# Performance work log

Measured on AMD Instinct MI355X. Metric: run time of the kernel, lower is better.

Reference implementation:

```python
import jax, jax.numpy as jnp
import numpy as np

NUM_HEADS = 16
D_MODEL = 2048
HEAD_DIM = 128
ROPE_BASE = 10000


def setup_inputs() -> dict:
    key = jax.random.key(0)
    k1, k2, k3 = jax.random.split(key, 3)
    B, S = 2, 2048
    x = jax.random.normal(k1, (B, S, D_MODEL), dtype=jnp.float32)
    attn_mask = jnp.ones((B, S), dtype=jnp.int32)
    in_proj = 0.02 * jax.random.normal(k2, (3, D_MODEL, NUM_HEADS, HEAD_DIM), dtype=jnp.float32)
    out_proj = 0.02 * jax.random.normal(k3, (NUM_HEADS, HEAD_DIM, D_MODEL), dtype=jnp.float32)
    return {"x": x, "attn_mask": attn_mask, "in_proj": in_proj, "out_proj": out_proj}


def _rope(t, seq_len):
    # t: [B, S, H, hd]; faithful to RotaryEmbedding.__call__ (concat layout, not interleaved)
    half = HEAD_DIM // 2
    inv_freq = 1.0 / (ROPE_BASE ** (2 * jnp.arange(0, half, dtype=jnp.float32) / HEAD_DIM))
    positions = jnp.arange(seq_len, dtype=jnp.float32)
    angles = positions[:, None] * inv_freq[None, :]            # [S, hd/2]
    cos = jnp.cos(angles)[None, :, None, :]                    # [1, S, 1, hd/2]
    sin = jnp.sin(angles)[None, :, None, :]
    tr = t.reshape(*t.shape[:-1], half, 2)                     # [B,S,H,hd/2,2]
    t0, t1 = tr[..., 0], tr[..., 1]
    out = jnp.concatenate([t0 * cos - t1 * sin, t0 * sin + t1 * cos], axis=-1)
    return out.reshape(t.shape)


def reference(x, attn_mask, in_proj, out_proj):
    B, S, D = x.shape
    qkv = jnp.einsum('bsd,tdhm->tbshm', x, in_proj)            # fused QKV
    q, k, v = qkv[0], qkv[1], qkv[2]
    q = _rope(q, S)
    k = _rope(k, S)
    q = jnp.einsum('bshd->bhsd', q)
    k = jnp.einsum('bshd->bhsd', k)
    v = jnp.einsum('bshd->bhsd', v)
    scores = jnp.einsum('bhqd,bhkd->bhqk', q, k) / jnp.sqrt(jnp.float32(HEAD_DIM))
    # causal mask * key padding mask, with diagonal forced to 1
    causal = jnp.tril(jnp.ones((S, S), dtype=scores.dtype))    # [S,S]
    key_mask = attn_mask.astype(scores.dtype)[:, None, :]      # [B,1,S]
    combined = causal[None, :, :] * key_mask                   # [B,S,S]
    eye = jnp.eye(S, dtype=bool)
    combined = jnp.where(eye[None, :, :], jnp.asarray(1.0, scores.dtype), combined)
    scores = scores + (-(1.0 - combined) * 1e9)[:, None, :, :]  # broadcast over heads
    attn_weights = jax.nn.softmax(scores, axis=-1)
    return jnp.einsum('bhqk,bhkd,hdo->bqo', attn_weights, v, out_proj)
```

## Files before the change

kernel.cpp:

```cpp
#include <hip/hip_runtime.h>
#include <hip/hip_bf16.h>

#define B_   2
#define S_   2048
#define H_   16
#define HD_  128
#define D_   2048
#define BS_  4096
#define SCALE_ 0.08838834764831845f

typedef __hip_bfloat16 bf16;
typedef float f32x4 __attribute__((ext_vector_type(4)));
typedef __bf16 bf16x8 __attribute__((ext_vector_type(8)));
typedef unsigned short u16x8 __attribute__((ext_vector_type(8)));
typedef unsigned short u16x4 __attribute__((ext_vector_type(4)));

static __device__ __forceinline__ unsigned short f2bf_u(float f) {
  bf16 h = __float2bfloat16(f);
  return __builtin_bit_cast(unsigned short, h);
}
static __device__ __forceinline__ void load_lds16(const void* g, void* l) {
  __builtin_amdgcn_global_load_lds((const __attribute__((address_space(1))) void*)g,
                                   (__attribute__((address_space(3))) void*)l, 16, 0, 0);
}

__global__ __launch_bounds__(256) void k_convert(const float* __restrict__ src,
                                                 bf16* __restrict__ dst) {
  const size_t i = ((size_t)blockIdx.x * 256 + threadIdx.x) * 8;
  const float4 a = *(const float4*)(src + i);
  const float4 b = *(const float4*)(src + i + 4);
  u16x8 o;
  o[0] = f2bf_u(a.x); o[1] = f2bf_u(a.y); o[2] = f2bf_u(a.z); o[3] = f2bf_u(a.w);
  o[4] = f2bf_u(b.x); o[5] = f2bf_u(b.y); o[6] = f2bf_u(b.z); o[7] = f2bf_u(b.w);
  *(u16x8*)(dst + i) = o;
}

__global__ __launch_bounds__(256) void k_transpose(const float* __restrict__ src0,
                                                   bf16* __restrict__ dst0) {
  const int z = blockIdx.z;
  const float* src = src0 + (size_t)z * D_ * D_;
  bf16* dst = dst0 + (size_t)z * D_ * D_;
  __shared__ float tile[64][65];
  const int t = threadIdx.x;
  const int x0 = blockIdx.x * 64, y0 = blockIdx.y * 64;
#pragma unroll
  for (int i = 0; i < 16; ++i) {
    int idx = t + i * 256, r = idx >> 6, c = idx & 63;
    tile[r][c] = src[(size_t)(y0 + r) * D_ + x0 + c];
  }
  __syncthreads();
#pragma unroll
  for (int i = 0; i < 16; ++i) {
    int idx = t + i * 256, c = idx >> 6, r = idx & 63;
    dst[(size_t)(x0 + c) * D_ + y0 + r] = __float2bfloat16(tile[r][c]);
  }
}

__global__ __launch_bounds__(256) void k_rope_tables(float* __restrict__ cost,
                                                     float* __restrict__ sint) {
  const int idx = blockIdx.x * 256 + threadIdx.x;
  const int s = idx >> 6, d = idx & 63;
  const float inv = expf(-(float)d * (9.210340371976184f / 64.f));
  const float ang = (float)s * inv;
  cost[idx] = cosf(ang);
  sint[idx] = sinf(ang);
}

template <int MODE>
__global__ __launch_bounds__(512, 4) void k_gemm_p(const bf16* __restrict__ A,
                                                   const bf16* __restrict__ Bt,
                                                   float* __restrict__ Cf,
                                                   bf16* __restrict__ qb,
                                                   bf16* __restrict__ kb,
                                                   bf16* __restrict__ vt,
                                                   const float* __restrict__ cost,
                                                   const float* __restrict__ sint) {
  constexpr int BN = (MODE == 1) ? 128 : 256;
  constexpr int NF = BN / 64;
  constexpr int BSTRIDE = 8192 + BN * 64;
  extern __shared__ __align__(16) char smem[];
  const int tid = threadIdx.x;
  const int w = tid >> 6, lane = tid & 63;
  const int wm = w >> 2, wn = w & 3;
  const int lr = lane & 15, lg = lane >> 4;
  const int brow = blockIdx.x * 128, bcol = blockIdx.y * BN;

  f32x4 acc[4][NF] = {};

  auto stage = [&](int kt, int buf) {
    char* base = smem + buf * BSTRIDE;
    {
      const int row = tid >> 2, su = tid & 3;
      const int up = su ^ ((row >> 1) & 3);
      load_lds16(A + (size_t)(brow + row) * D_ + kt * 32 + up * 8, base + w * 1024);
    }
#pragma unroll
    for (int i = 0; i < BN / 128; ++i) {
      const int slot = i * 512 + tid;
      const int row = slot >> 2, su = slot & 3;
      const int up = su ^ ((row >> 1) & 3);
      load_lds16(Bt + (size_t)(bcol + row) * D_ + kt * 32 + up * 8,
                 base + 8192 + i * 8192 + w * 1024);
    }
  };

  const int NKT = D_ / 32;
  stage(0, 0); stage(1, 1);
  int bs = 0;
  for (int kt = 0; kt < NKT; ++kt) {
    if (kt < NKT - 1) {
      if constexpr (MODE == 1) asm volatile("s_waitcnt vmcnt(2)" ::: "memory");
      else                     asm volatile("s_waitcnt vmcnt(3)" ::: "memory");
    } else {
      asm volatile("s_waitcnt vmcnt(0)" ::: "memory");
    }
    __builtin_amdgcn_s_barrier();
    __builtin_amdgcn_sched_barrier(0);
    if (kt + 2 < NKT) {
      int sb = bs + 2; if (sb >= 3) sb -= 3;
      stage(kt + 2, sb);
    }

    const char* base = smem + bs * BSTRIDE;
    bf16x8 af[4], bf4[NF];
#pragma unroll
    for (int q = 0; q < 4; ++q) {
      const int r = wm * 64 + q * 16 + lr;
      af[q] = *(const bf16x8*)(base + r * 64 + ((lg ^ ((r >> 1) & 3)) * 16));
    }
#pragma unroll
    for (int nf = 0; nf < NF; ++nf) {
      const int r = wn * (NF * 16) + nf * 16 + lr;
      bf4[nf] = *(const bf16x8*)(base + 8192 + r * 64 + ((lg ^ ((r >> 1) & 3)) * 16));
    }
    __builtin_amdgcn_s_setprio(1);
#pragma unroll
    for (int q = 0; q < 4; ++q)
#pragma unroll
      for (int nf = 0; nf < NF; ++nf)
        acc[q][nf] = __builtin_amdgcn_mfma_f32_16x16x32_bf16(af[q], bf4[nf], acc[q][nf], 0, 0, 0);
    __builtin_amdgcn_s_setprio(0);
    bs = (bs == 2) ? 0 : bs + 1;
  }

  if (MODE == 1) {
#pragma unroll
    for (int mf = 0; mf < 4; ++mf)
#pragma unroll
      for (int nf = 0; nf < NF; ++nf) {
        const int col = bcol + wn * (NF * 16) + nf * 16 + lr;
#pragma unroll
        for (int j = 0; j < 4; ++j) {
          const int row = brow + wm * 64 + mf * 16 + lg * 4 + j;
          Cf[(size_t)row * D_ + col] = acc[mf][nf][j];
        }
      }
  } else {
    const int t = bcol >> 11;
#pragma unroll
    for (int mf = 0; mf < 4; ++mf)
#pragma unroll
      for (int nf = 0; nf < NF; ++nf) {
        const int col = bcol + wn * (NF * 16) + nf * 16 + lr;
        const int h = (col >> 7) & (H_ - 1), mm = col & (HD_ - 1);
        if (t == 2) {
          const int row0 = brow + wm * 64 + mf * 16 + lg * 4;
          const int b = row0 >> 11, s0 = row0 & (S_ - 1);
          u16x4 pk;
#pragma unroll
          for (int j = 0; j < 4; ++j) pk[j] = f2bf_u(acc[mf][nf][j]);
          *(u16x4*)(vt + ((size_t)(b * H_ + h) * HD_ + mm) * S_ + s0) = pk;
        } else {
          const int i2 = mm >> 1;
          const bool odd = mm & 1;
#pragma unroll
          for (int j = 0; j < 4; ++j) {
            const int row = brow + wm * 64 + mf * 16 + lg * 4 + j;
            const int b = row >> 11, s = row & (S_ - 1);
            const float val = acc[mf][nf][j];
            const float part = __shfl_xor(val, 1, 64);
            const float c = cost[s * 64 + i2];
            const float sn = sint[s * 64 + i2];
            float o = odd ? (part * sn + val * c) : (val * c - part * sn);
            if (t == 0) o *= SCALE_;
            const int om = odd ? (64 + i2) : i2;
            bf16* dst = (t == 1) ? kb : qb;
            dst[((size_t)(b * H_ + h) * S_ + s) * HD_ + om] = __float2bfloat16(o);
          }
        }
      }
  }
}

__global__ __launch_bounds__(512, 4) void k_attn(const bf16* __restrict__ qb,
                                                 const bf16* __restrict__ kb,
                                                 const bf16* __restrict__ vt,
                                                 const int* __restrict__ mask,
                                                 bf16* __restrict__ attn_b) {
  const int tid = threadIdx.x, w = tid >> 6, lane = tid & 63;
  const int lr = lane & 15, lg = lane >> 4;
  const int qt = (blockIdx.y < 16) ? ((int)gridDim.x - 1 - (int)blockIdx.x)
                                   : (int)blockIdx.x;
  const int q0 = qt * 128;
  const int bh = blockIdx.y;
  const int b = bh >> 4, h = bh & (H_ - 1);
  const bf16* qp = qb + (size_t)bh * S_ * HD_;
  const bf16* kp = kb + (size_t)bh * S_ * HD_;
  const bf16* vp = vt + (size_t)bh * HD_ * S_;
  __shared__ __align__(16) bf16 Ks[2][64 * 128];
  __shared__ __align__(16) bf16 Vs[2][128 * 64];
  __shared__ __align__(16) bf16 Ps[8][16][40];

  const int qrow = q0 + w * 16 + lr;
  bf16x8 qf[4];
#pragma unroll
  for (int ks = 0; ks < 4; ++ks)
    qf[ks] = *(const bf16x8*)(qp + (size_t)qrow * HD_ + ks * 32 + lg * 8);

  float m_run[4], l_run[4];
  f32x4 oacc[8];
#pragma unroll
  for (int j = 0; j < 4; ++j) { m_run[j] = -INFINITY; l_run[j] = 0.f; }
#pragma unroll
  for (int c = 0; c < 8; ++c) oacc[c] = (f32x4)(0.f);

  auto stage = [&](int buf, int k0) {
#pragma unroll
    for (int i = 0; i < 2; ++i) {
      const int slot = i * 512 + tid;
      const int row = slot >> 4, j16 = slot & 15;
      load_lds16(kp + (size_t)(k0 + row) * HD_ + ((j16 ^ (row & 7)) * 8),
                 (char*)&Ks[buf][0] + i * 8192 + w * 1024);
    }
#pragma unroll
    for (int i = 0; i < 2; ++i) {
      const int slot = i * 512 + tid;
      const int row = slot >> 3, j8 = slot & 7;
      load_lds16(vp + (size_t)row * S_ + k0 + ((j8 ^ (row & 7)) * 8),
                 (char*)&Vs[buf][0] + i * 8192 + w * 1024);
    }
  };

  const int nt = 2 * qt + 2;
  stage(0, 0);
  asm volatile("s_waitcnt vmcnt(0)" ::: "memory");
  __syncthreads();

  int cur = 0;
  for (int it = 0; it < nt; ++it) {
    const int k0 = it * 64;
    if (it + 1 < nt) stage(cur ^ 1, k0 + 64);

    const bool active = (it + 1 < nt) || (w >= 4);

    if (active) {
      int mk4[4];
#pragma unroll
      for (int n = 0; n < 4; ++n) mk4[n] = mask[b * S_ + k0 + n * 16 + lr];

      const bf16* ksb = &Ks[cur][0];
      const bf16* vsb = &Vs[cur][0];

      f32x4 sacc[4] = {};
      __builtin_amdgcn_s_setprio(1);
#pragma unroll
      for (int n = 0; n < 4; ++n) {
        const int krow = n * 16 + lr;
#pragma unroll
        for (int ks = 0; ks < 4; ++ks) {
          const int j16 = (ks * 4 + lg) ^ (krow & 7);
          const bf16x8 kf = *(const bf16x8*)(ksb + krow * 128 + j16 * 8);
          sacc[n] = __builtin_amdgcn_mfma_f32_16x16x32_bf16(qf[ks], kf, sacc[n], 0, 0, 0);
        }
      }
      __builtin_amdgcn_s_setprio(0);

      float mblk[4] = {-INFINITY, -INFINITY, -INFINITY, -INFINITY};
#pragma unroll
      for (int n = 0; n < 4; ++n) {
        const int kcol = k0 + n * 16 + lr;
#pragma unroll
        for (int j = 0; j < 4; ++j) {
          const int r = q0 + w * 16 + lg * 4 + j;
          float sv = sacc[n][j];
          const bool allowed = (kcol <= r) && (mk4[n] != 0 || kcol == r);
          sv = allowed ? sv : -1e9f;
          sacc[n][j] = sv;
          mblk[j] = fmaxf(mblk[j], sv);
        }
      }
#pragma unroll
      for (int xm = 1; xm < 16; xm <<= 1)
#pragma unroll
        for (int j = 0; j < 4; ++j)
          mblk[j] = fmaxf(mblk[j], __shfl_xor(mblk[j], xm, 64));

      bool grow = false;
#pragma unroll
      for (int j = 0; j < 4; ++j) grow = grow || (mblk[j] > m_run[j] + 8.f);
      if (__any(grow)) {
        float alpha[4];
#pragma unroll
        for (int j = 0; j < 4; ++j) {
          const float mn = fmaxf(m_run[j], mblk[j]);
          alpha[j] = __expf(m_run[j] - mn);
          m_run[j] = mn;
          l_run[j] *= alpha[j];
        }
#pragma unroll
        for (int c = 0; c < 8; ++c)
#pragma unroll
          for (int j = 0; j < 4; ++j) oacc[c][j] *= alpha[j];
      }

      float psum[4] = {0.f, 0.f, 0.f, 0.f};
#pragma unroll
      for (int n = 0; n < 4; ++n)
#pragma unroll
        for (int j = 0; j < 4; ++j) {
          const float p = __expf(sacc[n][j] - m_run[j]);
          psum[j] += p;
          sacc[n][j] = p;
        }
#pragma unroll
      for (int xm = 1; xm < 16; xm <<= 1)
#pragma unroll
        for (int j = 0; j < 4; ++j)
          psum[j] += __shfl_xor(psum[j], xm, 64);
#pragma unroll
      for (int j = 0; j < 4; ++j) l_run[j] += psum[j];

#pragma unroll
      for (int hh = 0; hh < 2; ++hh) {
#pragma unroll
        for (int n2 = 0; n2 < 2; ++n2)
#pragma unroll
          for (int j = 0; j < 4; ++j)
            Ps[w][lg * 4 + j][n2 * 16 + lr] = __float2bfloat16(sacc[hh * 2 + n2][j]);
        const bf16x8 pa = *(const bf16x8*)(&Ps[w][lr][lg * 8]);
        __builtin_amdgcn_s_setprio(1);
#pragma unroll
        for (int c = 0; c < 8; ++c) {
          const int vrow = c * 16 + lr;
          const int unit = (hh * 4 + lg) ^ (vrow & 7);
          const bf16x8 vf = *(const bf16x8*)(vsb + vrow * 64 + unit * 8);
          oacc[c] = __builtin_amdgcn_mfma_f32_16x16x32_bf16(pa, vf, oacc[c], 0, 0, 0);
        }
        __builtin_amdgcn_s_setprio(0);
      }
    }

    asm volatile("s_waitcnt vmcnt(0)" ::: "memory");
    __syncthreads();
    cur ^= 1;
  }

#pragma unroll
  for (int j = 0; j < 4; ++j) {
    const float inv = 1.f / l_run[j];
    const int r = q0 + w * 16 + lg * 4 + j;
#pragma unroll
    for (int c = 0; c < 8; ++c)
      attn_b[(size_t)(b * S_ + r) * D_ + h * HD_ + c * 16 + lr] =
          __float2bfloat16(oacc[c][j] * inv);
  }
}

extern "C" void kernel_launch(void* const* d_in, const int* in_sizes, int n_in,
                              void* d_out, int out_size, void* d_ws, size_t ws_size,
                              hipStream_t stream) {
  (void)in_sizes; (void)n_in; (void)out_size; (void)ws_size;
  const float* x        = (const float*)d_in[0];
  const int*   attn_mask= (const int*)d_in[1];
  const float* in_proj  = (const float*)d_in[2];
  const float* out_proj = (const float*)d_in[3];
  float* out = (float*)d_out;
  char* ws = (char*)d_ws;

  bf16*  xb    = (bf16*)(ws + 0);
  bf16*  wqkvT = (bf16*)(ws + 16777216);
  bf16*  woT   = (bf16*)(ws + 41943040);
  float* cost  = (float*)(ws + 50331648);
  float* sint  = (float*)(ws + 50855936);
  bf16*  vt    = (bf16*)(ws + 51380224);
  bf16* qb = (bf16*)d_out;
  bf16* kb = (bf16*)((char*)d_out + 16777216);
  bf16* attn_b = xb;

  static int lds_ok = 0;
  if (!lds_ok) {
    (void)hipFuncSetAttribute((const void*)k_gemm_p<0>,
                              hipFuncAttributeMaxDynamicSharedMemorySize, 73728);
    (void)hipFuncSetAttribute((const void*)k_gemm_p<1>,
                              hipFuncAttributeMaxDynamicSharedMemorySize, 49152);
    lds_ok = 1;
  }

  k_convert<<<4096, 256, 0, stream>>>(x, xb);
  k_transpose<<<dim3(32, 32, 3), 256, 0, stream>>>(in_proj, wqkvT);
  k_transpose<<<dim3(32, 32, 1), 256, 0, stream>>>(out_proj, woT);
  k_rope_tables<<<512, 256, 0, stream>>>(cost, sint);
  k_gemm_p<0><<<dim3(32, 24), 512, 73728, stream>>>(xb, wqkvT, nullptr, qb, kb, vt, cost, sint);
  k_attn<<<dim3(16, 32), 512, 0, stream>>>(qb, kb, vt, attn_mask, attn_b);
  k_gemm_p<1><<<dim3(32, 16), 512, 49152, stream>>>(attn_b, woT, out, nullptr, nullptr, nullptr,
                                                    nullptr, nullptr);
}
```

Before: 278.5 us.

## Fuse prep kernels, remap GEMM workgroups across XCDs, use raw barriers in attention

Folds the convert, two transpose and rope-table kernels into one launch that picks its sub-task by block index, removing three launch gaps. The GEMM maps its flat workgroup index so that consecutive tiles land on the same XCD, aiming for better L2 reuse of A and B tiles. The attention loop swaps __syncthreads for a raw s_barrier plus sched_barrier, which avoids the implicit waitcnt and keeps the compiler from moving code across the barrier. The fused prep kernel uses shared memory for every block, including the convert and rope branches that never touch it, which could lower occupancy for those branches.

Measured after the change: 286.6 us. +2.9%, slower.

```diff
diff --git a/kernel.cpp b/kernel.cpp
--- a/kernel.cpp
+++ b/kernel.cpp
@@ -24,46 +24,58 @@
                                    (__attribute__((address_space(3))) void*)l, 16, 0, 0);
 }
 
-__global__ __launch_bounds__(256) void k_convert(const float* __restrict__ src,
-                                                 bf16* __restrict__ dst) {
-  const size_t i = ((size_t)blockIdx.x * 256 + threadIdx.x) * 8;
-  const float4 a = *(const float4*)(src + i);
-  const float4 b = *(const float4*)(src + i + 4);
-  u16x8 o;
-  o[0] = f2bf_u(a.x); o[1] = f2bf_u(a.y); o[2] = f2bf_u(a.z); o[3] = f2bf_u(a.w);
-  o[4] = f2bf_u(b.x); o[5] = f2bf_u(b.y); o[6] = f2bf_u(b.z); o[7] = f2bf_u(b.w);
-  *(u16x8*)(dst + i) = o;
-}
-
-__global__ __launch_bounds__(256) void k_transpose(const float* __restrict__ src0,
-                                                   bf16* __restrict__ dst0) {
-  const int z = blockIdx.z;
-  const float* src = src0 + (size_t)z * D_ * D_;
-  bf16* dst = dst0 + (size_t)z * D_ * D_;
+__global__ __launch_bounds__(256) void k_prep(const float* __restrict__ x,
+                                              bf16* __restrict__ xb,
+                                              const float* __restrict__ in_proj,
+                                              bf16* __restrict__ wqkvT,
+                                              const float* __restrict__ out_proj,
+                                              bf16* __restrict__ woT,
+                                              float* __restrict__ cost,
+                                              float* __restrict__ sint) {
   __shared__ float tile[64][65];
+  const int bid = blockIdx.x;
   const int t = threadIdx.x;
-  const int x0 = blockIdx.x * 64, y0 = blockIdx.y * 64;
-#pragma unroll
-  for (int i = 0; i < 16; ++i) {
-    int idx = t + i * 256, r = idx >> 6, c = idx & 63;
-    tile[r][c] = src[(size_t)(y0 + r) * D_ + x0 + c];
-  }
-  __syncthreads();
-#pragma unroll
-  for (int i = 0; i < 16; ++i) {
-    int idx = t + i * 256, c = idx >> 6, r = idx & 63;
-    dst[(size_t)(x0 + c) * D_ + y0 + r] = __float2bfloat16(tile[r][c]);
-  }
-}
-
-__global__ __launch_bounds__(256) void k_rope_tables(float* __restrict__ cost,
-                                                     float* __restrict__ sint) {
-  const int idx = blockIdx.x * 256 + threadIdx.x;
-  const int s = idx >> 6, d = idx & 63;
-  const float inv = expf(-(float)d * (9.210340371976184f / 64.f));
-  const float ang = (float)s * inv;
-  cost[idx] = cosf(ang);
-  sint[idx] = sinf(ang);
+  if (bid < 4096) {
+    const size_t i = ((size_t)bid * 256 + t) * 8;
+    const float4 a = *(const float4*)(x + i);
+    const float4 b = *(const float4*)(x + i + 4);
+    u16x8 o;
+    o[0] = f2bf_u(a.x); o[1] = f2bf_u(a.y); o[2] = f2bf_u(a.z); o[3] = f2bf_u(a.w);
+    o[4] = f2bf_u(b.x); o[5] = f2bf_u(b.y); o[6] = f2bf_u(b.z); o[7] = f2bf_u(b.w);
+    *(u16x8*)(xb + i) = o;
+  } else if (bid < 8192) {
+    const int local = bid - 4096;
+    const float* src;
+    bf16* dst;
+    if (local < 3072) {
+      const int z = local >> 10;
+      src = in_proj + (size_t)z * D_ * D_;
+      dst = wqkvT + (size_t)z * D_ * D_;
+    } else {
+      src = out_proj;
+      dst = woT;
+    }
+    const int rem = local & 1023;
+    const int x0 = (rem & 31) * 64, y0 = (rem >> 5) * 64;
+#pragma unroll
+    for (int i = 0; i < 16; ++i) {
+      int idx = t + i * 256, r = idx >> 6, c = idx & 63;
+      tile[r][c] = src[(size_t)(y0 + r) * D_ + x0 + c];
+    }
+    __syncthreads();
+#pragma unroll
+    for (int i = 0; i < 16; ++i) {
+      int idx = t + i * 256, c = idx >> 6, r = idx & 63;
+      dst[(size_t)(x0 + c) * D_ + y0 + r] = __float2bfloat16(tile[r][c]);
+    }
+  } else {
+    const int idx = (bid - 8192) * 256 + t;
+    const int s = idx >> 6, d = idx & 63;
+    const float inv = expf(-(float)d * (9.210340371976184f / 64.f));
+    const float ang = (float)s * inv;
+    cost[idx] = cosf(ang);
+    sint[idx] = sinf(ang);
+  }
 }
 
 template <int MODE>
@@ -83,7 +95,10 @@
   const int w = tid >> 6, lane = tid & 63;
   const int wm = w >> 2, wn = w & 3;
   const int lr = lane & 15, lg = lane >> 4;
-  const int brow = blockIdx.x * 128, bcol = blockIdx.y * BN;
+  const int nwg = 32 * (int)gridDim.y;
+  int f = (int)blockIdx.x + 32 * (int)blockIdx.y;
+  f = (f & 7) * (nwg >> 3) + (f >> 3);
+  const int brow = (f & 31) * 128, bcol = (f >> 5) * BN;
 
   f32x4 acc[4][NF] = {};
 
@@ -244,7 +259,8 @@
   const int nt = 2 * qt + 2;
   stage(0, 0);
   asm volatile("s_waitcnt vmcnt(0)" ::: "memory");
-  __syncthreads();
+  __builtin_amdgcn_s_barrier();
+  __builtin_amdgcn_sched_barrier(0);
 
   int cur = 0;
   for (int it = 0; it < nt; ++it) {
@@ -351,7 +367,8 @@
     }
 
     asm volatile("s_waitcnt vmcnt(0)" ::: "memory");
-    __syncthreads();
+    __builtin_amdgcn_s_barrier();
+    __builtin_amdgcn_sched_barrier(0);
     cur ^= 1;
   }
 
@@ -396,10 +413,7 @@
     lds_ok = 1;
   }
 
-  k_convert<<<4096, 256, 0, stream>>>(x, xb);
-  k_transpose<<<dim3(32, 32, 3), 256, 0, stream>>>(in_proj, wqkvT);
-  k_transpose<<<dim3(32, 32, 1), 256, 0, stream>>>(out_proj, woT);
-  k_rope_tables<<<512, 256, 0, stream>>>(cost, sint);
+  k_prep<<<8704, 256, 0, stream>>>(x, xb, in_proj, wqkvT, out_proj, woT, cost, sint);
   k_gemm_p<0><<<dim3(32, 24), 512, 73728, stream>>>(xb, wqkvT, nullptr, qb, kb, vt, cost, sint);
   k_attn<<<dim3(16, 32), 512, 0, stream>>>(qb, kb, vt, attn_mask, attn_b);
   k_gemm_p<1><<<dim3(32, 16), 512, 49152, stream>>>(attn_b, woT, out, nullptr, nullptr, nullptr,
```
